# Performance work log

Measured on AMD Instinct MI355X. Metric: run time of the kernel, lower is better.

Reference implementation:

```python
import jax, jax.numpy as jnp
import numpy as np

B, C, D, H, W = 1, 32, 48, 64, 208
EPS = 1e-5  # BatchNorm eps


def setup_inputs() -> dict:
    key = jax.random.key(0)
    ks = jax.random.split(key, 8)
    x = jax.random.normal(ks[0], (B, C, D, H, W), jnp.float32)
    g = jax.random.normal(ks[1], (B, 20, H, W), jnp.float32)
    conv_w = jax.random.normal(ks[2], (C, C, 3, 3, 3), jnp.float32) * 0.02
    bn1_gamma = 1.0 + 0.1 * jax.random.normal(ks[3], (C,), jnp.float32)
    bn1_beta = 0.1 * jax.random.normal(ks[4], (C,), jnp.float32)
    bn1_mean = 0.1 * jax.random.normal(ks[5], (C,), jnp.float32)
    bn1_var = jax.random.uniform(ks[6], (C,), jnp.float32, 0.5, 1.5)
    bn2_gamma = 1.0 + 0.1 * jax.random.normal(ks[7], (C,), jnp.float32)
    bn2_beta = jnp.zeros((C,), jnp.float32)
    bn2_mean = jnp.zeros((C,), jnp.float32)
    bn2_var = jnp.ones((C,), jnp.float32)
    return {
        'x': x, 'g': g, 'conv_w': conv_w,
        'bn1_gamma': bn1_gamma, 'bn1_beta': bn1_beta, 'bn1_mean': bn1_mean, 'bn1_var': bn1_var,
        'bn2_gamma': bn2_gamma, 'bn2_beta': bn2_beta, 'bn2_mean': bn2_mean, 'bn2_var': bn2_var,
    }


def _l1_normalize(k):
    # F.normalize(k, p=1, dim=1)
    return k / jnp.maximum(jnp.sum(jnp.abs(k), axis=1, keepdims=True), 1e-12)


def _sga_scan(x, w):
    """Directional semi-global aggregation along the LAST axis.
    x: [B,C,D,H,L] cost volume, w: [B,5,H,L] L1-normalized guidance weights.
    Recurrence (GANet SGA):
      A[p,d] = w0*x[p,d] + w1*A[p-1,d] + w2*A[p-1,d-1] + w3*A[p-1,d+1] + w4*max_d' A[p-1,d']
    """
    xs = jnp.moveaxis(x, -1, 0)  # [L,B,C,D,H]
    ws = jnp.moveaxis(w, -1, 0)  # [L,B,5,H]

    def step(prev, inp):
        xi, wi = inp  # [B,C,D,H], [B,5,H]
        w0, w1, w2, w3, w4 = [wi[:, i][:, None, None, :] for i in range(5)]
        up = jnp.concatenate([prev[:, :, :1], prev[:, :, :-1]], axis=2)   # A[d-1]
        dn = jnp.concatenate([prev[:, :, 1:], prev[:, :, -1:]], axis=2)   # A[d+1]
        mx = jnp.max(prev, axis=2, keepdims=True)                          # max_d A
        out = w0 * xi + w1 * prev + w2 * up + w3 * dn + w4 * mx
        return out, out

    _, outs = jax.lax.scan(step, xs[0], (xs, ws))  # boundary: carry init = raw cost slice
    return jnp.moveaxis(outs, 0, -1)


def _sga(x, k1, k2, k3, k4):
    # direction 1: left -> right (along W)
    d1 = _sga_scan(x, k1)
    # direction 2: right -> left
    d2 = jnp.flip(_sga_scan(jnp.flip(x, -1), jnp.flip(k2, -1)), -1)
    # vertical directions: swap H<->W so the scan axis is H
    xv = jnp.swapaxes(x, 3, 4)  # [B,C,D,W,H]
    d3 = jnp.swapaxes(_sga_scan(xv, jnp.swapaxes(k3, 2, 3)), 3, 4)  # top -> bottom
    d4 = jnp.swapaxes(
        jnp.flip(_sga_scan(jnp.flip(xv, -1), jnp.flip(jnp.swapaxes(k4, 2, 3), -1)), -1), 3, 4)
    # GANet combines directions with an elementwise max
    return jnp.maximum(jnp.maximum(d1, d2), jnp.maximum(d3, d4))


def _bn3d(x, gamma, beta, mean, var):
    s = (gamma / jnp.sqrt(var + EPS))[None, :, None, None, None]
    return (x - mean[None, :, None, None, None]) * s + beta[None, :, None, None, None]


def _conv3d_same(x, w):
    return jax.lax.conv_general_dilated(
        x, w, window_strides=(1, 1, 1), padding=[(1, 1)] * 3,
        dimension_numbers=('NCDHW', 'OIDHW', 'NCDHW'))


def reference(x, g, conv_w, bn1_gamma, bn1_beta, bn1_mean, bn1_var,
              bn2_gamma, bn2_beta, bn2_mean, bn2_var):
    rem = x
    k1, k2, k3, k4 = jnp.split(g, 4, axis=1)  # each [B,5,H,W]
    k1, k2, k3, k4 = map(_l1_normalize, (k1, k2, k3, k4))
    a = _sga(x, k1, k2, k3, k4)
    # refine=True branch: BN+ReLU then BasicConv(3x3x3, BN, no relu)
    a = jax.nn.relu(_bn3d(a, bn1_gamma, bn1_beta, bn1_mean, bn1_var))
    a = _conv3d_same(a, conv_w)
    a = _bn3d(a, bn2_gamma, bn2_beta, bn2_mean, bn2_var)
    return jax.nn.relu(a + rem)
```

## Files before the change

### kernel.cpp

```cpp
#include <hip/hip_runtime.h>
#include <hip/hip_bf16.h>
#include <cstddef>

#define C_ 32
#define D_ 48
#define DP_ 50
#define H_ 64
#define W_ 208
#define WP_ 210
#define HW_ 13312
#define HS_ 9984
#define EPS_ 1e-5f

typedef __attribute__((ext_vector_type(8))) short short8;
typedef __attribute__((ext_vector_type(4))) float float4v;
typedef __attribute__((ext_vector_type(16))) float float16v;
typedef __attribute__((ext_vector_type(2))) __fp16 half2v;

template<int CTRL>
__device__ __forceinline__ float dppmov(float x) {
    int v = __builtin_bit_cast(int, x);
    return __builtin_bit_cast(float,
        __builtin_amdgcn_update_dpp(v, v, CTRL, 0xf, 0xf, false));
}
template<int CTRL>
__device__ __forceinline__ float dppmax(float m) {
    return fmaxf(m, dppmov<CTRL>(m));
}
__device__ __forceinline__ float rl(float v, int idx) {
    return __builtin_bit_cast(float,
        __builtin_amdgcn_readlane(__builtin_bit_cast(int, v), idx));
}

__device__ __forceinline__ float sga_step_dpp(float A, float xi,
    float w0, float w1, float w2, float w3, float w4, bool actv, bool ge47)
{
    float up = dppmov<0x138>(A);
    float dn = dppmov<0x130>(A);
    dn = ge47 ? A : dn;
    float m = actv ? A : -3.4e38f;
    m = dppmax<0x111>(m);
    m = dppmax<0x112>(m);
    m = dppmax<0x114>(m);
    m = dppmax<0x118>(m);
    m = dppmax<0x142>(m);
    m = dppmax<0x143>(m);
    float mall = rl(m, 63);
    return (w0*xi + w1*A) + ((w2*up + w3*dn) + w4*mall);
}

__global__ __launch_bounds__(256) void prep_kernel(
    const float* __restrict__ g, const float* __restrict__ cw,
    float* __restrict__ wn, float* __restrict__ wnT,
    __hip_bfloat16* __restrict__ wrep, unsigned* __restrict__ actu)
{
    int idx = blockIdx.x * 256 + threadIdx.x;
    if (idx < 4 * HW_) {
        int dir = idx / HW_;
        int hw  = idx % HW_;
        const float* gb = g + dir * 5 * HW_ + hw;
        float v0 = gb[0*HW_], v1 = gb[1*HW_], v2 = gb[2*HW_], v3 = gb[3*HW_], v4 = gb[4*HW_];
        float s = fabsf(v0)+fabsf(v1)+fabsf(v2)+fabsf(v3)+fabsf(v4);
        float inv = 1.0f / fmaxf(s, 1e-12f);
        v0 *= inv; v1 *= inv; v2 *= inv; v3 *= inv; v4 *= inv;
        float* ob = wn + dir * 5 * HW_ + hw;
        ob[0*HW_] = v0; ob[1*HW_] = v1; ob[2*HW_] = v2; ob[3*HW_] = v3; ob[4*HW_] = v4;
        if (dir >= 2) {
            int hq = hw / W_, wq = hw % W_;
            float* oT = wnT + ((size_t)((dir-2)*5)*W_ + wq)*H_ + hq;
            oT[0]       = v0; oT[1*HW_] = v1; oT[2*HW_] = v2;
            oT[3*HW_]   = v3; oT[4*HW_] = v4;
        }
    } else if (idx < 4 * HW_ + 27648) {
        int j = idx - 4 * HW_;
        int e    = j & 7;
        int lane = (j >> 3) & 63;
        int q    = j >> 9;
        int cih  = q & 1;
        int tap  = q >> 1;
        int co = lane & 31;
        int ci = cih * 16 + (lane >> 5) * 8 + e;
        wrep[j] = __float2bfloat16(cw[(co * C_ + ci) * 27 + tap]);
    } else if (idx < 4 * HW_ + 27648 + 98304) {
        int j2 = idx - (4 * HW_ + 27648);
        int hd  = j2 >> 5;
        int r   = j2 & 31;
        int col = (r >> 4) ? 209 : 0;
        int cu  = r & 15;
        int h = hd / 48, dd = hd % 48;
        actu[(((size_t)h * DP_ + dd + 1) * WP_ + col) * 16 + cu] = 0u;
    } else {
        int j3 = idx - (4 * HW_ + 27648 + 98304);
        int pl   = j3 >= 215040;
        int r3   = pl ? j3 - 215040 : j3;
        int h    = r3 / 3360;
        int rest = r3 % 3360;
        int dpad = pl ? (DP_ - 1) : 0;
        actu[((size_t)h * DP_ + dpad) * WP_ * 16 + rest] = 0u;
    }
}

__global__ __launch_bounds__(256) void t0_kernel(
    const float* __restrict__ x, __hip_bfloat16* __restrict__ xt)
{
    __shared__ float t[48 * 257];
    int tid = threadIdx.x;
    int c  = blockIdx.x / 52;
    int q0 = (blockIdx.x % 52) * 256;
    #pragma unroll
    for (int dd = 0; dd < 48; ++dd)
        t[dd * 257 + tid] = x[((size_t)c * 48 + dd) * HW_ + q0 + tid];
    __syncthreads();
    unsigned* xtu = (unsigned*)xt;
    #pragma unroll
    for (int k = 0; k < 24; ++k) {
        int f = tid + 256 * k;
        int d2 = f % 24, hwl = f / 24;
        union { unsigned u; __hip_bfloat16 hh[2]; } pk;
        pk.hh[0] = __float2bfloat16(t[(2 * d2) * 257 + hwl]);
        pk.hh[1] = __float2bfloat16(t[(2 * d2 + 1) * 257 + hwl]);
        xtu[(((size_t)c * HW_ + q0 + hwl) * 48 + 2 * d2) >> 1] = pk.u;
    }
}

__global__ __launch_bounds__(256, 4) void sga_w_kernel(
    const __hip_bfloat16* __restrict__ xt, const float* __restrict__ wn,
    __hip_bfloat16* __restrict__ d12)
{
    __shared__ __fp16 sO[2][2][208][48];

    int lane = threadIdx.x & 63;
    int widb = threadIdx.x >> 6;
    int rowb = widb >> 1;
    int dir  = widb & 1;
    int grow = blockIdx.x * 2 + rowb;
    int c = grow >> 6, h = grow & 63;
    int d = lane < 48 ? lane : 47;
    bool actv = lane < 48, ge47 = lane >= 47;
    const __hip_bfloat16* xp = xt + ((size_t)c * HW_ + h * W_) * 48 + d;
    const float* wb = wn + (size_t)dir * 5 * HW_ + h * W_;
    int il = lane >> 3, jl = lane & 7;
    bool wact = il < 5;

    float xb[3][8];
    float wAr[3];

    if (dir == 0) {
        #pragma unroll
        for (int j = 0; j < 8; ++j) {
            xb[0][j] = __bfloat162float(xp[(size_t)j * 48]);
            xb[1][j] = __bfloat162float(xp[(size_t)(8 + j) * 48]);
        }
        wAr[0] = wact ? wb[il * HW_ + jl] : 0.0f;
        wAr[1] = wact ? wb[il * HW_ + 8 + jl] : 0.0f;
        float A = xb[0][0];
        #pragma unroll
        for (int cc = 0; cc < 26; ++cc) {
            const int buf = cc % 3;
            if (cc < 24) {
                const int nb = (cc + 2) % 3;
                #pragma unroll
                for (int j = 0; j < 8; ++j)
                    xb[nb][j] = __bfloat162float(xp[(size_t)((cc + 2) * 8 + j) * 48]);
                wAr[nb] = wact ? wb[il * HW_ + (cc + 2) * 8 + jl] : 0.0f;
            }
            #pragma unroll
            for (int j = 0; j < 8; ++j) {
                A = sga_step_dpp(A, xb[buf][j], rl(wAr[buf], j), rl(wAr[buf], 8 + j),
                                 rl(wAr[buf], 16 + j), rl(wAr[buf], 24 + j),
                                 rl(wAr[buf], 32 + j), actv, ge47);
                if (actv) sO[rowb][0][cc * 8 + j][d] = (__fp16)A;
            }
        }
    } else {
        #pragma unroll
        for (int j = 0; j < 8; ++j) {
            xb[0][j] = __bfloat162float(xp[(size_t)(200 + j) * 48]);
            xb[1][j] = __bfloat162float(xp[(size_t)(192 + j) * 48]);
        }
        wAr[0] = wact ? wb[il * HW_ + 200 + jl] : 0.0f;
        wAr[1] = wact ? wb[il * HW_ + 192 + jl] : 0.0f;
        float A = xb[0][7];
        #pragma unroll
        for (int cc2 = 0; cc2 < 26; ++cc2) {
            const int cc = 25 - cc2;
            const int buf = cc2 % 3;
            if (cc2 < 24) {
                const int nb = (cc2 + 2) % 3;
                #pragma unroll
                for (int j = 0; j < 8; ++j)
                    xb[nb][j] = __bfloat162float(xp[(size_t)((cc - 2) * 8 + j) * 48]);
                wAr[nb] = wact ? wb[il * HW_ + (cc - 2) * 8 + jl] : 0.0f;
            }
            #pragma unroll
            for (int j = 7; j >= 0; --j) {
                A = sga_step_dpp(A, xb[buf][j], rl(wAr[buf], j), rl(wAr[buf], 8 + j),
                                 rl(wAr[buf], 16 + j), rl(wAr[buf], 24 + j),
                                 rl(wAr[buf], 32 + j), actv, ge47);
                if (actv) sO[rowb][1][cc * 8 + j][d] = (__fp16)A;
            }
        }
    }

    __syncthreads();

    __hip_bfloat16* dp = d12 + ((size_t)c * HW_ + h * W_) * 48 + d;
    if (actv) {
        const int p0 = dir * 104;
        #pragma unroll
        for (int t = 0; t < 104; ++t) {
            int p = p0 + t;
            float d1 = (float)sO[rowb][0][p][d];
            float d2 = (float)sO[rowb][1][p][d];
            dp[(size_t)p * 48] = __float2bfloat16(fmaxf(d1, d2));
        }
    }
}

__global__ __launch_bounds__(256, 6) void sga_h_kernel(
    const __hip_bfloat16* __restrict__ xt, const float* __restrict__ wnT,
    __hip_bfloat16* __restrict__ d12,
    const float* __restrict__ g1, const float* __restrict__ b1,
    const float* __restrict__ m1, const float* __restrict__ v1)
{
    __shared__ __fp16 sA[2][2][64][48];

    int lane = threadIdx.x & 63;
    int widb = threadIdx.x >> 6;
    int colb = widb >> 1;
    int dir  = widb & 1;
    int gcol = blockIdx.x * 2 + colb;
    int c = gcol / W_, w = gcol % W_;
    int d = lane < 48 ? lane : 47;
    bool actv = lane < 48, ge47 = lane >= 47;
    const __hip_bfloat16* xp = xt + ((size_t)c * HW_ + w) * 48 + d;
    const float* wb = wnT + ((size_t)(dir * 5) * W_ + w) * H_;
    int il = lane >> 3, jl = lane & 7;
    bool wact = il < 5;

    float xb[3][8];
    float wAr[3];

    if (dir == 0) {
        #pragma unroll
        for (int j = 0; j < 8; ++j) {
            xb[0][j] = __bfloat162float(xp[(size_t)j * HS_]);
            xb[1][j] = __bfloat162float(xp[(size_t)(8 + j) * HS_]);
        }
        wAr[0] = wact ? wb[il * HW_ + jl] : 0.0f;
        wAr[1] = wact ? wb[il * HW_ + 8 + jl] : 0.0f;
        float A = xb[0][0];
        #pragma unroll
        for (int cc = 0; cc < 8; ++cc) {
            const int buf = cc % 3;
            if (cc < 6) {
                const int nb = (cc + 2) % 3;
                #pragma unroll
                for (int j = 0; j < 8; ++j)
                    xb[nb][j] = __bfloat162float(xp[(size_t)((cc + 2) * 8 + j) * HS_]);
                wAr[nb] = wact ? wb[il * HW_ + (cc + 2) * 8 + jl] : 0.0f;
            }
            #pragma unroll
            for (int j = 0; j < 8; ++j) {
                A = sga_step_dpp(A, xb[buf][j], rl(wAr[buf], j), rl(wAr[buf], 8 + j),
                                 rl(wAr[buf], 16 + j), rl(wAr[buf], 24 + j),
                                 rl(wAr[buf], 32 + j), actv, ge47);
                if (actv) sA[colb][0][cc * 8 + j][d] = (__fp16)A;
            }
        }
    } else {
        #pragma unroll
        for (int j = 0; j < 8; ++j) {
            xb[0][j] = __bfloat162float(xp[(size_t)(56 + j) * HS_]);
            xb[1][j] = __bfloat162float(xp[(size_t)(48 + j) * HS_]);
        }
        wAr[0] = wact ? wb[il * HW_ + 56 + jl] : 0.0f;
        wAr[1] = wact ? wb[il * HW_ + 48 + jl] : 0.0f;
        float A = xb[0][7];
        #pragma unroll
        for (int cc2 = 0; cc2 < 8; ++cc2) {
            const int cc = 7 - cc2;
            const int buf = cc2 % 3;
            if (cc2 < 6) {
                const int nb = (cc2 + 2) % 3;
                #pragma unroll
                for (int j = 0; j < 8; ++j)
                    xb[nb][j] = __bfloat162float(xp[(size_t)((cc - 2) * 8 + j) * HS_]);
                wAr[nb] = wact ? wb[il * HW_ + (cc - 2) * 8 + jl] : 0.0f;
            }
            #pragma unroll
            for (int j = 7; j >= 0; --j) {
                A = sga_step_dpp(A, xb[buf][j], rl(wAr[buf], j), rl(wAr[buf], 8 + j),
                                 rl(wAr[buf], 16 + j), rl(wAr[buf], 24 + j),
                                 rl(wAr[buf], 32 + j), actv, ge47);
                if (actv) sA[colb][1][cc * 8 + j][d] = (__fp16)A;
            }
        }
    }

    __syncthreads();

    float s1 = g1[c] * rsqrtf(v1[c] + EPS_);
    float o1 = b1[c] - m1[c] * s1;
    __hip_bfloat16* dp = d12 + ((size_t)c * HW_ + w) * 48 + d;
    #pragma unroll
    for (int t = 0; t < 32; ++t) {
        int h = dir * 32 + t;
        float dv = __bfloat162float(dp[(size_t)h * HS_]);
        float d3 = (float)sA[colb][0][h][d];
        float d4 = (float)sA[colb][1][h][d];
        float comb = fmaxf(fmaxf(d3, d4), dv);
        if (actv)
            dp[(size_t)h * HS_] = __float2bfloat16(fmaxf(comb * s1 + o1, 0.0f));
    }
}

__global__ __launch_bounds__(256) void trans_kernel(
    const __hip_bfloat16* __restrict__ st, __hip_bfloat16* __restrict__ act)
{
    __shared__ float t[8 * 1571];
    int tid = threadIdx.x;
    int h  = blockIdx.x / 26;
    int w0 = (blockIdx.x % 26) * 8;
    const unsigned* stu = (const unsigned*)st;
    #pragma unroll
    for (int k = 0; k < 24; ++k) {
        int f = tid + 256 * k;
        int d2 = f % 24, wl = (f / 24) % 8, c = f / 192;
        unsigned u = stu[(((size_t)c * HW_ + h * W_ + w0 + wl) * 48 + 2 * d2) >> 1];
        const __hip_bfloat16* bp = (const __hip_bfloat16*)&u;
        t[wl * 1571 + c * 49 + 2 * d2]     = __bfloat162float(bp[0]);
        t[wl * 1571 + c * 49 + 2 * d2 + 1] = __bfloat162float(bp[1]);
    }
    __syncthreads();
    unsigned* actu = (unsigned*)act;
    #pragma unroll
    for (int k = 0; k < 24; ++k) {
        int f = tid + 256 * k;
        int cp = f % 16, wl = (f / 16) % 8, d = f / 128;
        union { unsigned u; __hip_bfloat16 hh[2]; } pk;
        pk.hh[0] = __float2bfloat16(t[wl * 1571 + (2 * cp) * 49 + d]);
        pk.hh[1] = __float2bfloat16(t[wl * 1571 + (2 * cp + 1) * 49 + d]);
        actu[(((size_t)h * DP_ + d + 1) * WP_ + w0 + wl + 1) * 16 + cp] = pk.u;
    }
}

__global__ __launch_bounds__(256, 4) void conv_kernel(
    const __hip_bfloat16* __restrict__ act,
    const short8* __restrict__ wrep,
    const float* __restrict__ x,
    const float* __restrict__ g2, const float* __restrict__ b2,
    const float* __restrict__ m2, const float* __restrict__ v2,
    float* __restrict__ out)
{
    __shared__ __hip_bfloat16 sAct[10 * 34 * 40];

    int tid  = threadIdx.x;
    int lane = tid & 63;
    int v    = tid >> 6;
    int bid  = blockIdx.x;
    int wt   = bid % 7;
    int t    = bid / 7;
    int h    = t & 63;
    int d0b  = (t >> 6) * 8;
    int w0   = wt * 32;
    int n    = lane & 31;
    int half = lane >> 5;

    float16v acc0 = (float16v)(0.0f);
    float16v acc1 = (float16v)(0.0f);

    const short8* ap8 = (const short8*)act;

    #pragma unroll
    for (int kh = 0; kh < 3; ++kh) {
        int hh = h + kh - 1;
        if (hh < 0 || hh >= H_) continue;
        __syncthreads();
        #pragma unroll
        for (int k = 0; k < 6; ++k) {
            int i = tid + 256 * k;
            if (i < 1360) {
                int dp = i / 136;
                int r  = i - dp * 136;
                int wl = r >> 2, q = r & 3;
                int wc = w0 + wl; wc = wc < 209 ? wc : 209;
                short8 vd = ap8[(((size_t)hh * DP_ + d0b + dp) * WP_ + wc) * 4 + q];
                *(short8*)&sAct[(dp * 34 + wl) * 40 + q * 8] = vd;
            }
        }
        __syncthreads();
        #pragma unroll
        for (int kw = 0; kw < 3; ++kw) {
            #pragma unroll
            for (int cih = 0; cih < 2; ++cih) {
                short8 af[3];
                #pragma unroll
                for (int kd = 0; kd < 3; ++kd)
                    af[kd] = wrep[(((kd*3 + kh)*3 + kw)*2 + cih)*64 + lane];
                short8 bf[4];
                #pragma unroll
                for (int p = 0; p < 4; ++p)
                    bf[p] = *(const short8*)
                        &sAct[((2*v + p) * 34 + kw + n) * 40 + cih * 16 + half * 8];
                #pragma unroll
                for (int kd = 0; kd < 3; ++kd) {
                    acc0 = __builtin_amdgcn_mfma_f32_32x32x16_bf16(af[kd], bf[kd],   acc0, 0, 0, 0);
                    acc1 = __builtin_amdgcn_mfma_f32_32x32x16_bf16(af[kd], bf[kd+1], acc1, 0, 0, 0);
                }
            }
        }
    }

    int d0 = d0b + 2 * v;
    int wl = w0 + n;
    bool wvalid = wl < W_;
    int coh = 4 * half;
    #pragma unroll
    for (int r = 0; r < 16; ++r) {
        int co = (r & 3) + 8 * (r >> 2) + coh;
        float s2 = g2[co] * rsqrtf(v2[co] + EPS_);
        float o2 = b2[co] - m2[co] * s2;
        size_t idx0 = ((size_t)(co * D_ + d0) * H_ + h) * W_ + wl;
        if (wvalid) {
            out[idx0]       = fmaxf(acc0[r] * s2 + o2 + x[idx0],       0.0f);
            out[idx0 + HW_] = fmaxf(acc1[r] * s2 + o2 + x[idx0 + HW_], 0.0f);
        }
    }
}

extern "C" void kernel_launch(void* const* d_in, const int* in_sizes, int n_in,
                              void* d_out, int out_size, void* d_ws, size_t ws_size,
                              hipStream_t stream)
{
    const float* x    = (const float*)d_in[0];
    const float* g    = (const float*)d_in[1];
    const float* cw   = (const float*)d_in[2];
    const float* bn1g = (const float*)d_in[3];
    const float* bn1b = (const float*)d_in[4];
    const float* bn1m = (const float*)d_in[5];
    const float* bn1v = (const float*)d_in[6];
    const float* bn2g = (const float*)d_in[7];
    const float* bn2b = (const float*)d_in[8];
    const float* bn2m = (const float*)d_in[9];
    const float* bn2v = (const float*)d_in[10];
    float* out = (float*)d_out;

    char* ws = (char*)d_ws;
    float* wn  = (float*)ws;
    float* wnT = (float*)(ws + 1064960);
    __hip_bfloat16* wrep = (__hip_bfloat16*)(ws + 1597440);
    __hip_bfloat16* d12t = (__hip_bfloat16*)(ws + 1652736);
    __hip_bfloat16* act  = (__hip_bfloat16*)(ws + 42547200);
    __hip_bfloat16* xt = (__hip_bfloat16*)out;

    prep_kernel<<<2380, 256, 0, stream>>>(g, cw, wn, wnT, wrep, (unsigned*)act);
    t0_kernel<<<1664, 256, 0, stream>>>(x, xt);
    sga_w_kernel<<<1024, 256, 0, stream>>>(xt, wn, d12t);
    sga_h_kernel<<<3328, 256, 0, stream>>>(xt, wnT, d12t, bn1g, bn1b, bn1m, bn1v);
    trans_kernel<<<1664, 256, 0, stream>>>(d12t, act);
    conv_kernel<<<2688, 256, 0, stream>>>(act, (const short8*)wrep, x,
                                          bn2g, bn2b, bn2m, bn2v, out);
}
```

Baseline: 411.9 us.

## Pack two columns per wave in vertical SGA scan using packed fp16 math

The vertical (H-direction) SGA kernel now processes two adjacent W columns per wavefront. It packs their cost values and weights into half2 registers and runs the recurrence with packed fp16 arithmetic and v_pk_max_f16 for the disparity max. This halves the serial DPP/readlane chain per column and the number of waves launched, with blocks shrinking from 256 to 128 threads. The trade-off is that the scan accumulates in fp16 rather than fp32, which risks larger numerical error, and each wave has a longer load phase because it reads two columns.

```diff
diff --git a/kernel.cpp b/kernel.cpp
--- a/kernel.cpp
+++ b/kernel.cpp
@@ -31,6 +31,20 @@
     return __builtin_bit_cast(float,
         __builtin_amdgcn_readlane(__builtin_bit_cast(int, v), idx));
 }
+template<int CTRL>
+__device__ __forceinline__ unsigned dppu(unsigned x) {
+    return (unsigned)__builtin_amdgcn_update_dpp((int)x, (int)x, CTRL, 0xf, 0xf, false);
+}
+__device__ __forceinline__ unsigned rlu(unsigned v, int idx) {
+    return (unsigned)__builtin_amdgcn_readlane((int)v, idx);
+}
+__device__ __forceinline__ unsigned pkmax_u(unsigned a, unsigned b) {
+    unsigned r;
+    asm("v_pk_max_f16 %0, %1, %2" : "=v"(r) : "v"(a), "v"(b));
+    return r;
+}
+__device__ __forceinline__ half2v hcast(unsigned u) { return __builtin_bit_cast(half2v, u); }
+__device__ __forceinline__ unsigned ucast(half2v h) { return __builtin_bit_cast(unsigned, h); }
 
 __device__ __forceinline__ float sga_step_dpp(float A, float xi,
     float w0, float w1, float w2, float w3, float w4, bool actv, bool ge47)
@@ -47,6 +61,28 @@
     m = dppmax<0x143>(m);
     float mall = rl(m, 63);
     return (w0*xi + w1*A) + ((w2*up + w3*dn) + w4*mall);
+}
+
+__device__ __forceinline__ unsigned sga_step_pk(unsigned Au, unsigned xiu,
+    unsigned w0, unsigned w1, unsigned w2, unsigned w3, unsigned w4,
+    bool actv, bool ge47)
+{
+    unsigned up = dppu<0x138>(Au);
+    unsigned dn = dppu<0x130>(Au);
+    dn = ge47 ? Au : dn;
+    unsigned m = actv ? Au : 0xFBFFFBFFu;
+    m = pkmax_u(m, dppu<0x111>(m));
+    m = pkmax_u(m, dppu<0x112>(m));
+    m = pkmax_u(m, dppu<0x114>(m));
+    m = pkmax_u(m, dppu<0x118>(m));
+    m = pkmax_u(m, dppu<0x142>(m));
+    m = pkmax_u(m, dppu<0x143>(m));
+    unsigned mall = rlu(m, 63);
+    half2v A = hcast(Au), xi = hcast(xiu), uph = hcast(up), dnh = hcast(dn),
+           mh = hcast(mall), h0 = hcast(w0), h1 = hcast(w1), h2 = hcast(w2),
+           h3 = hcast(w3), h4 = hcast(w4);
+    half2v r = (h0 * xi + h1 * A) + ((h2 * uph + h3 * dnh) + h4 * mh);
+    return ucast(r);
 }
 
 __global__ __launch_bounds__(256) void prep_kernel(
@@ -217,66 +253,83 @@
     }
 }
 
-__global__ __launch_bounds__(256, 6) void sga_h_kernel(
+__global__ __launch_bounds__(128, 3) void sga_h_kernel(
     const __hip_bfloat16* __restrict__ xt, const float* __restrict__ wnT,
     __hip_bfloat16* __restrict__ d12,
     const float* __restrict__ g1, const float* __restrict__ b1,
     const float* __restrict__ m1, const float* __restrict__ v1)
 {
-    __shared__ __fp16 sA[2][2][64][48];
+    __shared__ unsigned sO[2][64][48];
 
     int lane = threadIdx.x & 63;
-    int widb = threadIdx.x >> 6;
-    int colb = widb >> 1;
-    int dir  = widb & 1;
-    int gcol = blockIdx.x * 2 + colb;
-    int c = gcol / W_, w = gcol % W_;
+    int dir  = threadIdx.x >> 6;
+    int gp   = blockIdx.x;
+    int g0 = gp * 2;
+    int c = g0 / W_, w = g0 % W_;
     int d = lane < 48 ? lane : 47;
     bool actv = lane < 48, ge47 = lane >= 47;
-    const __hip_bfloat16* xp = xt + ((size_t)c * HW_ + w) * 48 + d;
-    const float* wb = wnT + ((size_t)(dir * 5) * W_ + w) * H_;
+    const __hip_bfloat16* xA = xt + ((size_t)c * HW_ + w) * 48 + d;
+    const __hip_bfloat16* xB = xA + 48;
+    const float* wbA = wnT + ((size_t)(dir * 5) * W_ + w) * H_;
+    const float* wbB = wbA + H_;
     int il = lane >> 3, jl = lane & 7;
     bool wact = il < 5;
 
-    float xb[3][8];
-    float wAr[3];
+    unsigned xpk[3][8];
+    unsigned wAr[3];
 
     if (dir == 0) {
         #pragma unroll
-        for (int j = 0; j < 8; ++j) {
-            xb[0][j] = __bfloat162float(xp[(size_t)j * HS_]);
-            xb[1][j] = __bfloat162float(xp[(size_t)(8 + j) * HS_]);
-        }
-        wAr[0] = wact ? wb[il * HW_ + jl] : 0.0f;
-        wAr[1] = wact ? wb[il * HW_ + 8 + jl] : 0.0f;
-        float A = xb[0][0];
+        for (int b = 0; b < 2; ++b) {
+            #pragma unroll
+            for (int j = 0; j < 8; ++j) {
+                float fA = __bfloat162float(xA[(size_t)(b * 8 + j) * HS_]);
+                float fB = __bfloat162float(xB[(size_t)(b * 8 + j) * HS_]);
+                xpk[b][j] = ucast(__builtin_amdgcn_cvt_pkrtz(fA, fB));
+            }
+            float wfA = wact ? wbA[il * HW_ + b * 8 + jl] : 0.0f;
+            float wfB = wact ? wbB[il * HW_ + b * 8 + jl] : 0.0f;
+            wAr[b] = ucast(__builtin_amdgcn_cvt_pkrtz(wfA, wfB));
+        }
+        unsigned Au = xpk[0][0];
         #pragma unroll
         for (int cc = 0; cc < 8; ++cc) {
             const int buf = cc % 3;
             if (cc < 6) {
                 const int nb = (cc + 2) % 3;
                 #pragma unroll
-                for (int j = 0; j < 8; ++j)
-                    xb[nb][j] = __bfloat162float(xp[(size_t)((cc + 2) * 8 + j) * HS_]);
-                wAr[nb] = wact ? wb[il * HW_ + (cc + 2) * 8 + jl] : 0.0f;
+                for (int j = 0; j < 8; ++j) {
+                    float fA = __bfloat162float(xA[(size_t)((cc + 2) * 8 + j) * HS_]);
+                    float fB = __bfloat162float(xB[(size_t)((cc + 2) * 8 + j) * HS_]);
+                    xpk[nb][j] = ucast(__builtin_amdgcn_cvt_pkrtz(fA, fB));
+                }
+                float wfA = wact ? wbA[il * HW_ + (cc + 2) * 8 + jl] : 0.0f;
+                float wfB = wact ? wbB[il * HW_ + (cc + 2) * 8 + jl] : 0.0f;
+                wAr[nb] = ucast(__builtin_amdgcn_cvt_pkrtz(wfA, wfB));
             }
             #pragma unroll
             for (int j = 0; j < 8; ++j) {
-                A = sga_step_dpp(A, xb[buf][j], rl(wAr[buf], j), rl(wAr[buf], 8 + j),
-                                 rl(wAr[buf], 16 + j), rl(wAr[buf], 24 + j),
-                                 rl(wAr[buf], 32 + j), actv, ge47);
-                if (actv) sA[colb][0][cc * 8 + j][d] = (__fp16)A;
+                Au = sga_step_pk(Au, xpk[buf][j], rlu(wAr[buf], j), rlu(wAr[buf], 8 + j),
+                                 rlu(wAr[buf], 16 + j), rlu(wAr[buf], 24 + j),
+                                 rlu(wAr[buf], 32 + j), actv, ge47);
+                if (actv) sO[0][cc * 8 + j][d] = Au;
             }
         }
     } else {
         #pragma unroll
-        for (int j = 0; j < 8; ++j) {
-            xb[0][j] = __bfloat162float(xp[(size_t)(56 + j) * HS_]);
-            xb[1][j] = __bfloat162float(xp[(size_t)(48 + j) * HS_]);
-        }
-        wAr[0] = wact ? wb[il * HW_ + 56 + jl] : 0.0f;
-        wAr[1] = wact ? wb[il * HW_ + 48 + jl] : 0.0f;
-        float A = xb[0][7];
+        for (int b = 0; b < 2; ++b) {
+            const int base = 56 - b * 8;
+            #pragma unroll
+            for (int j = 0; j < 8; ++j) {
+                float fA = __bfloat162float(xA[(size_t)(base + j) * HS_]);
+                float fB = __bfloat162float(xB[(size_t)(base + j) * HS_]);
+                xpk[b][j] = ucast(__builtin_amdgcn_cvt_pkrtz(fA, fB));
+            }
+            float wfA = wact ? wbA[il * HW_ + base + jl] : 0.0f;
+            float wfB = wact ? wbB[il * HW_ + base + jl] : 0.0f;
+            wAr[b] = ucast(__builtin_amdgcn_cvt_pkrtz(wfA, wfB));
+        }
+        unsigned Au = xpk[0][7];
         #pragma unroll
         for (int cc2 = 0; cc2 < 8; ++cc2) {
             const int cc = 7 - cc2;
@@ -284,16 +337,21 @@
             if (cc2 < 6) {
                 const int nb = (cc2 + 2) % 3;
                 #pragma unroll
-                for (int j = 0; j < 8; ++j)
-                    xb[nb][j] = __bfloat162float(xp[(size_t)((cc - 2) * 8 + j) * HS_]);
-                wAr[nb] = wact ? wb[il * HW_ + (cc - 2) * 8 + jl] : 0.0f;
+                for (int j = 0; j < 8; ++j) {
+                    float fA = __bfloat162float(xA[(size_t)((cc - 2) * 8 + j) * HS_]);
+                    float fB = __bfloat162float(xB[(size_t)((cc - 2) * 8 + j) * HS_]);
+                    xpk[nb][j] = ucast(__builtin_amdgcn_cvt_pkrtz(fA, fB));
+                }
+                float wfA = wact ? wbA[il * HW_ + (cc - 2) * 8 + jl] : 0.0f;
+                float wfB = wact ? wbB[il * HW_ + (cc - 2) * 8 + jl] : 0.0f;
+                wAr[nb] = ucast(__builtin_amdgcn_cvt_pkrtz(wfA, wfB));
             }
             #pragma unroll
             for (int j = 7; j >= 0; --j) {
-                A = sga_step_dpp(A, xb[buf][j], rl(wAr[buf], j), rl(wAr[buf], 8 + j),
-                                 rl(wAr[buf], 16 + j), rl(wAr[buf], 24 + j),
-                                 rl(wAr[buf], 32 + j), actv, ge47);
-                if (actv) sA[colb][1][cc * 8 + j][d] = (__fp16)A;
+                Au = sga_step_pk(Au, xpk[buf][j], rlu(wAr[buf], j), rlu(wAr[buf], 8 + j),
+                                 rlu(wAr[buf], 16 + j), rlu(wAr[buf], 24 + j),
+                                 rlu(wAr[buf], 32 + j), actv, ge47);
+                if (actv) sO[1][cc * 8 + j][d] = Au;
             }
         }
     }
@@ -302,16 +360,19 @@
 
     float s1 = g1[c] * rsqrtf(v1[c] + EPS_);
     float o1 = b1[c] - m1[c] * s1;
-    __hip_bfloat16* dp = d12 + ((size_t)c * HW_ + w) * 48 + d;
+    __hip_bfloat16* dpA = d12 + ((size_t)c * HW_ + w) * 48 + d;
+    __hip_bfloat16* dpB = dpA + 48;
     #pragma unroll
     for (int t = 0; t < 32; ++t) {
         int h = dir * 32 + t;
-        float dv = __bfloat162float(dp[(size_t)h * HS_]);
-        float d3 = (float)sA[colb][0][h][d];
-        float d4 = (float)sA[colb][1][h][d];
-        float comb = fmaxf(fmaxf(d3, d4), dv);
-        if (actv)
-            dp[(size_t)h * HS_] = __float2bfloat16(fmaxf(comb * s1 + o1, 0.0f));
+        unsigned um = pkmax_u(sO[0][h][d], sO[1][h][d]);
+        half2v mh = hcast(um);
+        if (actv) {
+            float vA = fmaxf((float)mh[0], __bfloat162float(dpA[(size_t)h * HS_]));
+            float vB = fmaxf((float)mh[1], __bfloat162float(dpB[(size_t)h * HS_]));
+            dpA[(size_t)h * HS_] = __float2bfloat16(fmaxf(vA * s1 + o1, 0.0f));
+            dpB[(size_t)h * HS_] = __float2bfloat16(fmaxf(vB * s1 + o1, 0.0f));
+        }
     }
 }
 
@@ -457,7 +518,7 @@
     prep_kernel<<<2380, 256, 0, stream>>>(g, cw, wn, wnT, wrep, (unsigned*)act);
     t0_kernel<<<1664, 256, 0, stream>>>(x, xt);
     sga_w_kernel<<<1024, 256, 0, stream>>>(xt, wn, d12t);
-    sga_h_kernel<<<3328, 256, 0, stream>>>(xt, wnT, d12t, bn1g, bn1b, bn1m, bn1v);
+    sga_h_kernel<<<3328, 128, 0, stream>>>(xt, wnT, d12t, bn1g, bn1b, bn1m, bn1v);
     trans_kernel<<<1664, 256, 0, stream>>>(d12t, act);
     conv_kernel<<<2688, 256, 0, stream>>>(act, (const short8*)wrep, x,
                                           bn2g, bn2b, bn2m, bn2v, out);
```

Result: faster. 397.4 us (-3.5%).
